# Performance work log

Measured on AMD Instinct MI355X. Metric: run time of the kernel, lower is better.

The kernel has to match this reference:

```python
import jax, jax.numpy as jnp
import numpy as np

# ---- static config (from module __init__ defaults) ----
INPUT_DIM = 3
NUM_LEVELS = 16
LEVEL_DIM = 2
SCALE = 2.0
BASE_RES = 16
LOG2_T = 19
MAX_T = 2 ** LOG2_T
NUM_FREQS = 6
N_POINTS = 2_000_000
PRIMES = np.array([1, 2654435761, 805459861], dtype=np.uint32)  # Instant-NGP spatial hash primes
CORNERS = np.array([[i, j, k] for i in (0, 1) for j in (0, 1) for k in (0, 1)], dtype=np.int32)  # [8,3]

RES = [int(np.floor(BASE_RES * SCALE ** l)) for l in range(NUM_LEVELS)]
SIZES = [min(MAX_T, (r + 1) ** 3) for r in RES]  # dense if the full grid fits in the hashmap
OFFSETS = np.concatenate([[0], np.cumsum(SIZES)]).astype(np.int64)
TOTAL = int(OFFSETS[-1])  # 7,131,219 rows


def setup_inputs() -> dict:
    key = jax.random.key(0)
    k1, k2 = jax.random.split(key)
    x = jax.random.uniform(k1, (N_POINTS, INPUT_DIM), dtype=jnp.float32)  # points in [0,1]^3
    # hash-grid features init U(-1e-4, 1e-4) as in Instant-NGP
    table = (jax.random.uniform(k2, (TOTAL, LEVEL_DIM), dtype=jnp.float32) * 2.0 - 1.0) * 1e-4
    return {"x": x, "table": table}


def _level_interp(x, table_l, res, size):
    """Trilinear hash-grid interpolation at one level. x:[N,3] in [0,1]."""
    pos = x * jnp.float32(res)            # [N,3]
    p0f = jnp.floor(pos)
    frac = pos - p0f                      # [N,3]
    p0 = p0f.astype(jnp.int32)
    corners = jnp.clip(p0[:, None, :] + CORNERS[None], 0, res)  # [N,8,3], grid has res+1 verts
    if (res + 1) ** 3 <= MAX_T:
        # dense stride indexing
        r1 = res + 1
        idx = corners[..., 0] + corners[..., 1] * r1 + corners[..., 2] * (r1 * r1)
    else:
        c = corners.astype(jnp.uint32)
        h = (c[..., 0] * jnp.uint32(int(PRIMES[0]))
             ^ c[..., 1] * jnp.uint32(int(PRIMES[1]))
             ^ c[..., 2] * jnp.uint32(int(PRIMES[2])))
        idx = (h % jnp.uint32(size)).astype(jnp.int32)
    vals = table_l[idx]                   # [N,8,level_dim] gather
    # trilinear weights: prod over dims of (frac if corner==1 else 1-frac)
    w = jnp.where(CORNERS[None] == 1, frac[:, None, :], 1.0 - frac[:, None, :]).prod(-1)  # [N,8]
    return jnp.einsum('nc,ncd->nd', w, vals)  # [N,level_dim]


def _hash_encode(x, table):
    feats = [
        _level_interp(x, table[int(OFFSETS[l]):int(OFFSETS[l + 1])], RES[l], SIZES[l])
        for l in range(NUM_LEVELS)
    ]
    return jnp.concatenate(feats, axis=-1)  # [N, num_levels*level_dim]


def _pos_encode(x):
    coeffs = jnp.float32(2.0) ** jnp.arange(NUM_FREQS, dtype=jnp.float32)  # log_sampling
    xc = x[:, None, :] * coeffs[None, :, None]           # [N,F,3]
    sc = jnp.stack([jnp.sin(xc), jnp.cos(xc)], axis=2)   # [N,F,2,3] -> order: per-freq sin(3) then cos(3)
    return jnp.concatenate([x, sc.reshape(x.shape[0], 2 * NUM_FREQS * INPUT_DIM)], axis=-1)


def reference(x, table):
    hash_feat = _hash_encode(x, table)   # [N,32]
    freq_feat = _pos_encode(x)           # [N,39]
    return jnp.concatenate([hash_feat, freq_feat], axis=-1)  # [N,71]
```

## Files before the change

kernel.cpp:

```cpp
#include <hip/hip_runtime.h>

typedef float f4 __attribute__((ext_vector_type(4)));

#define BLK 128
#define NLEV 16
#define NHASH 13
#define HSIZE 524288
#define HMASK 524287u
#define KOFF3 315475

__constant__ int kOff[NLEV] = {0, 4913, 40850, 315475, 839763, 1364051, 1888339,
                               2412627, 2936915, 3461203, 3985491, 4509779,
                               5034067, 5558355, 6082643, 6606931};

__global__ __launch_bounds__(256)
void convert_kernel(const float2* __restrict__ tab, unsigned* __restrict__ tbf)
{
    const int i = blockIdx.x * 256 + threadIdx.x;
    if (i >= NHASH * HSIZE) return;
    float2 v = tab[KOFF3 + i];
    tbf[i] = (__float_as_uint(v.x) >> 16) | (__float_as_uint(v.y) & 0xFFFF0000u);
}

__global__ __launch_bounds__(256)
void levels_kernel(const float* __restrict__ xs, const unsigned* __restrict__ tbf,
                   unsigned* __restrict__ scratch, int n)
{
    const int lev = blockIdx.y;
    const int i0  = blockIdx.x * 512 + threadIdx.x;
    const int res = 16 << (3 + lev);
    const float fres = (float)res;
    const unsigned* __restrict__ tl = tbf + (size_t)lev * HSIZE;

    unsigned hx[2], hc[2][4];
    float rx[2], ry[2], rz[2];
    bool valid[2];

    #pragma unroll
    for (int p = 0; p < 2; ++p) {
        const int i = i0 + p * 256;
        valid[p] = (i < n);
        float px = 0.f, py = 0.f, pz = 0.f;
        if (valid[p]) {
            px = __builtin_nontemporal_load(&xs[3 * i + 0]);
            py = __builtin_nontemporal_load(&xs[3 * i + 1]);
            pz = __builtin_nontemporal_load(&xs[3 * i + 2]);
        }
        float posx = px * fres, posy = py * fres, posz = pz * fres;
        float fxf = floorf(posx), fyf = floorf(posy), fzf = floorf(posz);
        rx[p] = posx - fxf; ry[p] = posy - fyf; rz[p] = posz - fzf;
        unsigned x  = (unsigned)(int)fxf;
        unsigned y0 = (unsigned)(int)fyf * 2654435761u, y1 = y0 + 2654435761u;
        unsigned z0 = (unsigned)(int)fzf * 805459861u,  z1 = z0 + 805459861u;
        hx[p] = x;
        hc[p][0] = y0 ^ z0; hc[p][1] = y0 ^ z1; hc[p][2] = y1 ^ z0; hc[p][3] = y1 ^ z1;
    }

    unsigned va[2][4], vb[2][4];
    #pragma unroll
    for (int p = 0; p < 2; ++p) {
        #pragma unroll
        for (int c = 0; c < 4; ++c) {
            unsigned ia = (hx[p] ^ hc[p][c]) & HMASK;
            uint2 q = *(const uint2*)(tl + (ia & ~1u));
            va[p][c] = (ia & 1u) ? q.y : q.x;
            vb[p][c] = (ia & 1u) ? q.x : q.y;
        }
    }
    #pragma unroll
    for (int p = 0; p < 2; ++p) {
        if (hx[p] & 1u) {
            unsigned x1 = hx[p] + 1u;
            #pragma unroll
            for (int c = 0; c < 4; ++c)
                vb[p][c] = tl[(x1 ^ hc[p][c]) & HMASK];
        }
    }

    #pragma unroll
    for (int p = 0; p < 2; ++p) {
        if (!valid[p]) continue;
        float wx1 = rx[p], wx0 = 1.f - wx1;
        float wy1 = ry[p], wy0 = 1.f - wy1;
        float wz1 = rz[p], wz0 = 1.f - wz1;
        float wc[4] = {wy0 * wz0, wy0 * wz1, wy1 * wz0, wy1 * wz1};
        float f0 = 0.f, f1 = 0.f;
        #pragma unroll
        for (int c = 0; c < 4; ++c) {
            float a0 = __uint_as_float(va[p][c] << 16);
            float a1 = __uint_as_float(va[p][c] & 0xFFFF0000u);
            float b0 = __uint_as_float(vb[p][c] << 16);
            float b1 = __uint_as_float(vb[p][c] & 0xFFFF0000u);
            f0 += wc[c] * (wx0 * a0 + wx1 * b0);
            f1 += wc[c] * (wx0 * a1 + wx1 * b1);
        }
        unsigned packed = (__float_as_uint(f0) >> 16) | (__float_as_uint(f1) & 0xFFFF0000u);
        __builtin_nontemporal_store(packed, &scratch[(size_t)lev * n + (i0 + p * 256)]);
    }
}

__global__ __launch_bounds__(256)
void levels_f32_kernel(const float* __restrict__ xs, const float2* __restrict__ tab,
                       unsigned* __restrict__ scratch, int n)
{
    const int lev = blockIdx.y;
    const int i   = blockIdx.x * 256 + threadIdx.x;
    if (i >= n) return;
    const int res = 16 << (3 + lev);
    const float2* __restrict__ tl = tab + kOff[3 + lev];

    const float px = __builtin_nontemporal_load(&xs[3 * i + 0]);
    const float py = __builtin_nontemporal_load(&xs[3 * i + 1]);
    const float pz = __builtin_nontemporal_load(&xs[3 * i + 2]);

    const float fres = (float)res;
    float posx = px * fres, posy = py * fres, posz = pz * fres;
    float fxf = floorf(posx), fyf = floorf(posy), fzf = floorf(posz);
    float rx = posx - fxf, ry = posy - fyf, rz = posz - fzf;

    unsigned hx  = (unsigned)(int)fxf;
    unsigned hy0 = (unsigned)(int)fyf * 2654435761u, hy1 = hy0 + 2654435761u;
    unsigned hz0 = (unsigned)(int)fzf * 805459861u,  hz1 = hz0 + 805459861u;
    unsigned h00 = hy0 ^ hz0, h01 = hy0 ^ hz1, h10 = hy1 ^ hz0, h11 = hy1 ^ hz1;

    unsigned hx1 = hx + 1u;
    float2 v000 = tl[(hx ^ h00) & HMASK], v100 = tl[(hx1 ^ h00) & HMASK];
    float2 v001 = tl[(hx ^ h01) & HMASK], v101 = tl[(hx1 ^ h01) & HMASK];
    float2 v010 = tl[(hx ^ h10) & HMASK], v110 = tl[(hx1 ^ h10) & HMASK];
    float2 v011 = tl[(hx ^ h11) & HMASK], v111 = tl[(hx1 ^ h11) & HMASK];

    float wx1 = rx, wx0 = 1.f - rx;
    float wy1 = ry, wy0 = 1.f - ry;
    float wz1 = rz, wz0 = 1.f - rz;

    float f0, f1, w;
    w = wx0 * wy0 * wz0; f0  = w * v000.x; f1  = w * v000.y;
    w = wx0 * wy0 * wz1; f0 += w * v001.x; f1 += w * v001.y;
    w = wx0 * wy1 * wz0; f0 += w * v010.x; f1 += w * v010.y;
    w = wx0 * wy1 * wz1; f0 += w * v011.x; f1 += w * v011.y;
    w = wx1 * wy0 * wz0; f0 += w * v100.x; f1 += w * v100.y;
    w = wx1 * wy0 * wz1; f0 += w * v101.x; f1 += w * v101.y;
    w = wx1 * wy1 * wz0; f0 += w * v110.x; f1 += w * v110.y;
    w = wx1 * wy1 * wz1; f0 += w * v111.x; f1 += w * v111.y;

    unsigned packed = (__float_as_uint(f0) >> 16) | (__float_as_uint(f1) & 0xFFFF0000u);
    __builtin_nontemporal_store(packed, &scratch[(size_t)lev * n + i]);
}

__global__ __launch_bounds__(BLK)
void final_kernel(const float* __restrict__ xs, const float* __restrict__ table,
                  const unsigned* __restrict__ scratch, float* __restrict__ out, int n)
{
    __shared__ float sbuf[BLK * 71];
    const int tid  = threadIdx.x;
    const int base = blockIdx.x * BLK;
    const int pi   = base + tid;

    float px = 0.f, py = 0.f, pz = 0.f;
    if (pi < n) {
        px = xs[3 * pi + 0];
        py = xs[3 * pi + 1];
        pz = xs[3 * pi + 2];
    }

    float* srow = sbuf + tid * 71;
    const float2* __restrict__ tab = (const float2*)table;

    #pragma unroll
    for (int l = 0; l < 3; ++l) {
        const int res = 16 << l;
        const float2* __restrict__ tl = tab + kOff[l];
        const float fres = (float)res;

        float posx = px * fres, posy = py * fres, posz = pz * fres;
        float fxf = floorf(posx), fyf = floorf(posy), fzf = floorf(posz);
        float rx = posx - fxf, ry = posy - fyf, rz = posz - fzf;

        const unsigned r1 = (unsigned)(res + 1);
        const unsigned r2 = r1 * r1;
        unsigned x0 = (unsigned)(int)fxf;
        unsigned by0 = (unsigned)(int)fyf * r1; unsigned by1 = by0 + r1;
        unsigned cz0 = (unsigned)(int)fzf * r2; unsigned cz1 = cz0 + r2;

        float2 v000, v001, v010, v011, v100, v101, v110, v111;
        #define PAIRD(B, VA, VB) { \
            unsigned i0 = x0 + (B); \
            if ((i0 & 1u) == 0u) { f4 q = *(const f4*)(tl + i0); \
                VA.x = q.x; VA.y = q.y; VB.x = q.z; VB.y = q.w; } \
            else { VA = tl[i0]; VB = tl[i0 + 1u]; } }
        PAIRD(by0 + cz0, v000, v100)
        PAIRD(by0 + cz1, v001, v101)
        PAIRD(by1 + cz0, v010, v110)
        PAIRD(by1 + cz1, v011, v111)
        #undef PAIRD

        float wx1 = rx, wx0 = 1.f - rx;
        float wy1 = ry, wy0 = 1.f - ry;
        float wz1 = rz, wz0 = 1.f - rz;

        float f0, f1, w;
        w = wx0 * wy0 * wz0; f0  = w * v000.x; f1  = w * v000.y;
        w = wx0 * wy0 * wz1; f0 += w * v001.x; f1 += w * v001.y;
        w = wx0 * wy1 * wz0; f0 += w * v010.x; f1 += w * v010.y;
        w = wx0 * wy1 * wz1; f0 += w * v011.x; f1 += w * v011.y;
        w = wx1 * wy0 * wz0; f0 += w * v100.x; f1 += w * v100.y;
        w = wx1 * wy0 * wz1; f0 += w * v101.x; f1 += w * v101.y;
        w = wx1 * wy1 * wz0; f0 += w * v110.x; f1 += w * v110.y;
        w = wx1 * wy1 * wz1; f0 += w * v111.x; f1 += w * v111.y;

        srow[2 * l]     = f0;
        srow[2 * l + 1] = f1;
    }

    if (pi < n) {
        #pragma unroll
        for (int h = 0; h < NHASH; ++h) {
            unsigned u = __builtin_nontemporal_load(&scratch[(size_t)h * n + pi]);
            srow[6 + 2 * h] = __uint_as_float(u << 16);
            srow[7 + 2 * h] = __uint_as_float(u & 0xFFFF0000u);
        }
    }

    srow[32] = px; srow[33] = py; srow[34] = pz;
    float coef = 1.f;
    #pragma unroll
    for (int f = 0; f < 6; ++f) {
        float s, c;
        __sincosf(px * coef, &s, &c); srow[35 + 6*f + 0] = s; srow[35 + 6*f + 3] = c;
        __sincosf(py * coef, &s, &c); srow[35 + 6*f + 1] = s; srow[35 + 6*f + 4] = c;
        __sincosf(pz * coef, &s, &c); srow[35 + 6*f + 2] = s; srow[35 + 6*f + 5] = c;
        coef *= 2.f;
    }

    __syncthreads();

    const int nvalid = min(BLK, n - base);
    float* obase = out + (size_t)base * 71;
    if (nvalid == BLK) {
        f4* o4 = (f4*)obase;
        const f4* s4 = (const f4*)sbuf;
        #pragma unroll 1
        for (int i = tid; i < (BLK * 71) / 4; i += BLK)
            __builtin_nontemporal_store(s4[i], &o4[i]);
    } else {
        #pragma unroll 1
        for (int i = tid; i < nvalid * 71; i += BLK)
            __builtin_nontemporal_store(sbuf[i], &obase[i]);
    }
}

extern "C" void kernel_launch(void* const* d_in, const int* in_sizes, int n_in,
                              void* d_out, int out_size, void* d_ws, size_t ws_size,
                              hipStream_t stream) {
    const float* xs    = (const float*)d_in[0];
    const float* table = (const float*)d_in[1];
    float* out = (float*)d_out;
    const int n = in_sizes[0] / 3;

    unsigned* scratch = (unsigned*)d_ws;
    const size_t featBytes = (size_t)NHASH * (size_t)n * 4u;
    const size_t needBf16  = featBytes + (size_t)NHASH * HSIZE * 4u;
    const float2* tab = (const float2*)table;

    if (ws_size >= needBf16) {
        unsigned* tbf = (unsigned*)((char*)d_ws + featBytes);
        const int gc = (NHASH * HSIZE + 255) / 256;
        hipLaunchKernelGGL(convert_kernel, dim3(gc), dim3(256), 0, stream, tab, tbf);
        const int bpl = (n + 511) / 512;
        hipLaunchKernelGGL(levels_kernel, dim3(bpl, NHASH), dim3(256), 0, stream,
                           xs, tbf, scratch, n);
    } else {
        const int bpl = (n + 255) / 256;
        hipLaunchKernelGGL(levels_f32_kernel, dim3(bpl, NHASH), dim3(256), 0, stream,
                           xs, tab, scratch, n);
    }

    const int gf = (n + BLK - 1) / BLK;
    hipLaunchKernelGGL(final_kernel, dim3(gf), dim3(BLK), 0, stream,
                       xs, table, scratch, out, n);
}
```

Measured before the change: 892.6 us.

## Pack points into float4 once, prefetch scratch early, use double-angle sincos

Adds a prep kernel that converts the table to bf16 and also repacks xyz into 16-byte float4 rows, so the 13 level passes and the final pass each read points with one aligned vector load instead of three strided scalar loads. The final kernel issues its scratch loads before the dense-level interpolation so their latency overlaps that work. It also replaces six sincos calls per axis with one call plus double-angle recurrences. In exchange it writes and reads an extra float4 buffer, and the recurrence accumulates rounding error at higher frequencies.

```diff
diff --git a/kernel.cpp b/kernel.cpp
--- a/kernel.cpp
+++ b/kernel.cpp
@@ -8,22 +8,36 @@
 #define HSIZE 524288
 #define HMASK 524287u
 #define KOFF3 315475
+#define CONV_BLOCKS ((NHASH * HSIZE) / 256)
 
 __constant__ int kOff[NLEV] = {0, 4913, 40850, 315475, 839763, 1364051, 1888339,
                                2412627, 2936915, 3461203, 3985491, 4509779,
                                5034067, 5558355, 6082643, 6606931};
 
 __global__ __launch_bounds__(256)
-void convert_kernel(const float2* __restrict__ tab, unsigned* __restrict__ tbf)
-{
-    const int i = blockIdx.x * 256 + threadIdx.x;
-    if (i >= NHASH * HSIZE) return;
-    float2 v = tab[KOFF3 + i];
-    tbf[i] = (__float_as_uint(v.x) >> 16) | (__float_as_uint(v.y) & 0xFFFF0000u);
+void prep_kernel(const float* __restrict__ xs, const float2* __restrict__ tab,
+                 unsigned* __restrict__ tbf, f4* __restrict__ xs4, int n)
+{
+    const int b = blockIdx.x;
+    if (b < CONV_BLOCKS) {
+        const int i = b * 256 + threadIdx.x;
+        float2 v = tab[KOFF3 + i];
+        tbf[i] = (__float_as_uint(v.x) >> 16) | (__float_as_uint(v.y) & 0xFFFF0000u);
+    } else {
+        const int i = (b - CONV_BLOCKS) * 256 + threadIdx.x;
+        if (i < n) {
+            f4 p;
+            p.x = xs[3 * i + 0];
+            p.y = xs[3 * i + 1];
+            p.z = xs[3 * i + 2];
+            p.w = 0.f;
+            __builtin_nontemporal_store(p, &xs4[i]);
+        }
+    }
 }
 
 __global__ __launch_bounds__(256)
-void levels_kernel(const float* __restrict__ xs, const unsigned* __restrict__ tbf,
+void levels_kernel(const f4* __restrict__ xs4, const unsigned* __restrict__ tbf,
                    unsigned* __restrict__ scratch, int n)
 {
     const int lev = blockIdx.y;
@@ -40,13 +54,9 @@
     for (int p = 0; p < 2; ++p) {
         const int i = i0 + p * 256;
         valid[p] = (i < n);
-        float px = 0.f, py = 0.f, pz = 0.f;
-        if (valid[p]) {
-            px = __builtin_nontemporal_load(&xs[3 * i + 0]);
-            py = __builtin_nontemporal_load(&xs[3 * i + 1]);
-            pz = __builtin_nontemporal_load(&xs[3 * i + 2]);
-        }
-        float posx = px * fres, posy = py * fres, posz = pz * fres;
+        f4 pt = {0.f, 0.f, 0.f, 0.f};
+        if (valid[p]) pt = __builtin_nontemporal_load(&xs4[i]);
+        float posx = pt.x * fres, posy = pt.y * fres, posz = pt.z * fres;
         float fxf = floorf(posx), fyf = floorf(posy), fzf = floorf(posz);
         rx[p] = posx - fxf; ry[p] = posy - fyf; rz[p] = posz - fzf;
         unsigned x  = (unsigned)(int)fxf;
@@ -148,20 +158,25 @@
 }
 
 __global__ __launch_bounds__(BLK)
-void final_kernel(const float* __restrict__ xs, const float* __restrict__ table,
+void final_kernel(const f4* __restrict__ xs4, const float* __restrict__ table,
                   const unsigned* __restrict__ scratch, float* __restrict__ out, int n)
 {
     __shared__ float sbuf[BLK * 71];
     const int tid  = threadIdx.x;
     const int base = blockIdx.x * BLK;
     const int pi   = base + tid;
-
-    float px = 0.f, py = 0.f, pz = 0.f;
-    if (pi < n) {
-        px = xs[3 * pi + 0];
-        py = xs[3 * pi + 1];
-        pz = xs[3 * pi + 2];
-    }
+    const bool val = (pi < n);
+
+    unsigned sc[NHASH];
+    if (val) {
+        #pragma unroll
+        for (int h = 0; h < NHASH; ++h)
+            sc[h] = __builtin_nontemporal_load(&scratch[(size_t)h * n + pi]);
+    }
+
+    f4 pt = {0.f, 0.f, 0.f, 0.f};
+    if (val) pt = __builtin_nontemporal_load(&xs4[pi]);
+    const float px = pt.x, py = pt.y, pz = pt.z;
 
     float* srow = sbuf + tid * 71;
     const float2* __restrict__ tab = (const float2*)table;
@@ -212,24 +227,28 @@
         srow[2 * l + 1] = f1;
     }
 
-    if (pi < n) {
-        #pragma unroll
-        for (int h = 0; h < NHASH; ++h) {
-            unsigned u = __builtin_nontemporal_load(&scratch[(size_t)h * n + pi]);
-            srow[6 + 2 * h] = __uint_as_float(u << 16);
-            srow[7 + 2 * h] = __uint_as_float(u & 0xFFFF0000u);
-        }
+    #pragma unroll
+    for (int h = 0; h < NHASH; ++h) {
+        srow[6 + 2 * h] = __uint_as_float(sc[h] << 16);
+        srow[7 + 2 * h] = __uint_as_float(sc[h] & 0xFFFF0000u);
     }
 
     srow[32] = px; srow[33] = py; srow[34] = pz;
-    float coef = 1.f;
+    float sx, cx, sy, cy, sz, cz;
+    __sincosf(px, &sx, &cx);
+    __sincosf(py, &sy, &cy);
+    __sincosf(pz, &sz, &cz);
     #pragma unroll
     for (int f = 0; f < 6; ++f) {
-        float s, c;
-        __sincosf(px * coef, &s, &c); srow[35 + 6*f + 0] = s; srow[35 + 6*f + 3] = c;
-        __sincosf(py * coef, &s, &c); srow[35 + 6*f + 1] = s; srow[35 + 6*f + 4] = c;
-        __sincosf(pz * coef, &s, &c); srow[35 + 6*f + 2] = s; srow[35 + 6*f + 5] = c;
-        coef *= 2.f;
+        srow[35 + 6*f + 0] = sx; srow[35 + 6*f + 3] = cx;
+        srow[35 + 6*f + 1] = sy; srow[35 + 6*f + 4] = cy;
+        srow[35 + 6*f + 2] = sz; srow[35 + 6*f + 5] = cz;
+        if (f < 5) {
+            float nsx = 2.f * sx * cx, ncx = 1.f - 2.f * sx * sx;
+            float nsy = 2.f * sy * cy, ncy = 1.f - 2.f * sy * sy;
+            float nsz = 2.f * sz * cz, ncz = 1.f - 2.f * sz * sz;
+            sx = nsx; cx = ncx; sy = nsy; cy = ncy; sz = nsz; cz = ncz;
+        }
     }
 
     __syncthreads();
@@ -249,6 +268,83 @@
     }
 }
 
+__global__ __launch_bounds__(BLK)
+void final_f32_kernel(const float* __restrict__ xs, const float* __restrict__ table,
+                      const unsigned* __restrict__ scratch, float* __restrict__ out, int n)
+{
+    __shared__ float sbuf[BLK * 71];
+    const int tid  = threadIdx.x;
+    const int base = blockIdx.x * BLK;
+    const int pi   = base + tid;
+
+    float px = 0.f, py = 0.f, pz = 0.f;
+    if (pi < n) { px = xs[3*pi]; py = xs[3*pi+1]; pz = xs[3*pi+2]; }
+
+    float* srow = sbuf + tid * 71;
+    const float2* __restrict__ tab = (const float2*)table;
+
+    #pragma unroll
+    for (int l = 0; l < 3; ++l) {
+        const int res = 16 << l;
+        const float2* __restrict__ tl = tab + kOff[l];
+        const float fres = (float)res;
+        float posx = px * fres, posy = py * fres, posz = pz * fres;
+        float fxf = floorf(posx), fyf = floorf(posy), fzf = floorf(posz);
+        float rx = posx - fxf, ry = posy - fyf, rz = posz - fzf;
+        const unsigned r1 = (unsigned)(res + 1), r2 = r1 * r1;
+        unsigned x0 = (unsigned)(int)fxf;
+        unsigned by0 = (unsigned)(int)fyf * r1, by1 = by0 + r1;
+        unsigned cz0 = (unsigned)(int)fzf * r2, cz1 = cz0 + r2;
+        float2 v000 = tl[x0+by0+cz0], v100 = tl[x0+by0+cz0+1];
+        float2 v001 = tl[x0+by0+cz1], v101 = tl[x0+by0+cz1+1];
+        float2 v010 = tl[x0+by1+cz0], v110 = tl[x0+by1+cz0+1];
+        float2 v011 = tl[x0+by1+cz1], v111 = tl[x0+by1+cz1+1];
+        float wx1 = rx, wx0 = 1.f - rx, wy1 = ry, wy0 = 1.f - ry, wz1 = rz, wz0 = 1.f - rz;
+        float f0, f1, w;
+        w = wx0*wy0*wz0; f0  = w*v000.x; f1  = w*v000.y;
+        w = wx0*wy0*wz1; f0 += w*v001.x; f1 += w*v001.y;
+        w = wx0*wy1*wz0; f0 += w*v010.x; f1 += w*v010.y;
+        w = wx0*wy1*wz1; f0 += w*v011.x; f1 += w*v011.y;
+        w = wx1*wy0*wz0; f0 += w*v100.x; f1 += w*v100.y;
+        w = wx1*wy0*wz1; f0 += w*v101.x; f1 += w*v101.y;
+        w = wx1*wy1*wz0; f0 += w*v110.x; f1 += w*v110.y;
+        w = wx1*wy1*wz1; f0 += w*v111.x; f1 += w*v111.y;
+        srow[2*l] = f0; srow[2*l+1] = f1;
+    }
+    if (pi < n) {
+        #pragma unroll
+        for (int h = 0; h < NHASH; ++h) {
+            unsigned u = __builtin_nontemporal_load(&scratch[(size_t)h * n + pi]);
+            srow[6+2*h] = __uint_as_float(u << 16);
+            srow[7+2*h] = __uint_as_float(u & 0xFFFF0000u);
+        }
+    }
+    srow[32] = px; srow[33] = py; srow[34] = pz;
+    float coef = 1.f;
+    #pragma unroll
+    for (int f = 0; f < 6; ++f) {
+        float s, c;
+        __sincosf(px*coef, &s, &c); srow[35+6*f+0] = s; srow[35+6*f+3] = c;
+        __sincosf(py*coef, &s, &c); srow[35+6*f+1] = s; srow[35+6*f+4] = c;
+        __sincosf(pz*coef, &s, &c); srow[35+6*f+2] = s; srow[35+6*f+5] = c;
+        coef *= 2.f;
+    }
+    __syncthreads();
+    const int nvalid = min(BLK, n - base);
+    float* obase = out + (size_t)base * 71;
+    if (nvalid == BLK) {
+        f4* o4 = (f4*)obase;
+        const f4* s4 = (const f4*)sbuf;
+        #pragma unroll 1
+        for (int i = tid; i < (BLK * 71) / 4; i += BLK)
+            __builtin_nontemporal_store(s4[i], &o4[i]);
+    } else {
+        #pragma unroll 1
+        for (int i = tid; i < nvalid * 71; i += BLK)
+            __builtin_nontemporal_store(sbuf[i], &obase[i]);
+    }
+}
+
 extern "C" void kernel_launch(void* const* d_in, const int* in_sizes, int n_in,
                               void* d_out, int out_size, void* d_ws, size_t ws_size,
                               hipStream_t stream) {
@@ -259,23 +355,29 @@
 
     unsigned* scratch = (unsigned*)d_ws;
     const size_t featBytes = (size_t)NHASH * (size_t)n * 4u;
-    const size_t needBf16  = featBytes + (size_t)NHASH * HSIZE * 4u;
+    const size_t tblBytes  = (size_t)NHASH * HSIZE * 4u;
+    const size_t xs4Bytes  = (size_t)n * 16u;
     const float2* tab = (const float2*)table;
-
-    if (ws_size >= needBf16) {
+    const int gf = (n + BLK - 1) / BLK;
+
+    if (ws_size >= featBytes + tblBytes + xs4Bytes) {
         unsigned* tbf = (unsigned*)((char*)d_ws + featBytes);
-        const int gc = (NHASH * HSIZE + 255) / 256;
-        hipLaunchKernelGGL(convert_kernel, dim3(gc), dim3(256), 0, stream, tab, tbf);
+        f4* xs4 = (f4*)((char*)d_ws + featBytes + tblBytes);
+
+        const int packBlocks = (n + 255) / 256;
+        hipLaunchKernelGGL(prep_kernel, dim3(CONV_BLOCKS + packBlocks), dim3(256),
+                           0, stream, xs, tab, tbf, xs4, n);
+
         const int bpl = (n + 511) / 512;
         hipLaunchKernelGGL(levels_kernel, dim3(bpl, NHASH), dim3(256), 0, stream,
-                           xs, tbf, scratch, n);
+                           xs4, tbf, scratch, n);
+        hipLaunchKernelGGL(final_kernel, dim3(gf), dim3(BLK), 0, stream,
+                           xs4, table, scratch, out, n);
     } else {
         const int bpl = (n + 255) / 256;
         hipLaunchKernelGGL(levels_f32_kernel, dim3(bpl, NHASH), dim3(256), 0, stream,
                            xs, tab, scratch, n);
-    }
-
-    const int gf = (n + BLK - 1) / BLK;
-    hipLaunchKernelGGL(final_kernel, dim3(gf), dim3(BLK), 0, stream,
-                       xs, table, scratch, out, n);
-}
+        hipLaunchKernelGGL(final_f32_kernel, dim3(gf), dim3(BLK), 0, stream,
+                           xs, table, scratch, out, n);
+    }
+}
```

Measured after the change: 897.3 us. No clear change (+0.5%).
